# Performance work log

Measured on AMD Instinct MI355X. Metric: run time of the kernel, lower is better.

## Reference

```python
import jax, jax.numpy as jnp
import numpy as np

B, N, M, DK, DV, H = 4, 2048, 2048, 1024, 1024, 16
DKP = ((DK + H - 1) // H) * H  # 1024
DVP = ((DV + H - 1) // H) * H  # 1024


def setup_inputs() -> dict:
    key = jax.random.key(0)
    ks = jax.random.split(key, 12)
    s = 0.02
    return {
        "queries": jax.random.normal(ks[0], (B, N, DK), jnp.float32),
        "keys": jax.random.normal(ks[1], (B, M, DK), jnp.float32),
        "values": jax.random.normal(ks[2], (B, M, DV), jnp.float32),
        "presence": jnp.ones((B, M), jnp.float32),
        "n_heads": H,
        "wq": jax.random.normal(ks[3], (DK, DKP), jnp.float32) * s,
        "bq": jnp.zeros((DKP,), jnp.float32),
        "wk": jax.random.normal(ks[4], (DK, DKP), jnp.float32) * s,
        "bk": jnp.zeros((DKP,), jnp.float32),
        "wv": jax.random.normal(ks[5], (DV, DVP), jnp.float32) * s,
        "bv": jnp.zeros((DVP,), jnp.float32),
        "wo": jax.random.normal(ks[6], (DVP, DV), jnp.float32) * s,
        "bo": jnp.zeros((DV,), jnp.float32),
    }


def reference(queries, keys, values, presence, n_heads, wq, bq, wk, bk, wv, bv, wo, bo):
    b, n, _ = queries.shape
    m = keys.shape[1]
    h = n_heads
    # projections
    q = (queries @ wq + bq).reshape(b, n, h, -1)  # [B,N,H,dh]
    k = (keys @ wk + bk).reshape(b, m, h, -1)     # [B,M,H,dh]
    v = (values @ wv + bv).reshape(b, m, h, -1)   # [B,M,H,dv]
    dh = q.shape[-1]
    # scores: per-head scale is sqrt(per-head key dim), as in qkv_attention
    logits = jnp.einsum("bnhd,bmhd->bhnm", q, k)
    logits = logits - (1.0 - presence)[:, None, None, :] * 1e32
    attn = jax.nn.softmax(logits / jnp.sqrt(jnp.asarray(dh, logits.dtype)), axis=-1)
    o = jnp.einsum("bhnm,bmhd->bnhd", attn, v).reshape(b, n, -1)  # [B,N,DVP]
    return o @ wo + bo
```

## Files before the change

### kernel.cpp

```cpp
#include <hip/hip_runtime.h>


#define DI __device__ __forceinline__

typedef float f32x4 __attribute__((ext_vector_type(4)));
typedef __bf16 bf16x8 __attribute__((ext_vector_type(8)));
typedef __bf16 bf16x2 __attribute__((ext_vector_type(2)));
typedef unsigned short ushort8v __attribute__((ext_vector_type(8)));
typedef unsigned int uint4v __attribute__((ext_vector_type(4)));

typedef const __attribute__((address_space(1))) void gvoid_t;
typedef __attribute__((address_space(3))) void lvoid_t;

DI unsigned short f2b(float f) { return __builtin_bit_cast(unsigned short, (__bf16)f); }

DI unsigned pack2(float a, float b) {
  bf16x2 v;
  v[0] = (__bf16)a;
  v[1] = (__bf16)b;
  return __builtin_bit_cast(unsigned, v);
}

DI void swap32(unsigned& x, unsigned& y) {
  asm volatile("v_permlane32_swap_b32 %0, %1" : "+v"(x), "+v"(y));
}
DI void swap16(unsigned& x, unsigned& y) {
  asm volatile("v_permlane16_swap_b32 %0, %1" : "+v"(x), "+v"(y));
}

DI void gload16(const void* g, void* l) {
  __builtin_amdgcn_global_load_lds((gvoid_t*)g, (lvoid_t*)l, 16, 0, 0);
}

__global__ __launch_bounds__(256) void cvt3_kernel(const float* __restrict__ q,
                                                   const float* __restrict__ k,
                                                   const float* __restrict__ v,
                                                   unsigned short* __restrict__ qo,
                                                   unsigned short* __restrict__ ko,
                                                   unsigned short* __restrict__ vo) {
  const int z = blockIdx.y;
  const float* in = z == 0 ? q : z == 1 ? k : v;
  unsigned short* out = z == 0 ? qo : z == 1 ? ko : vo;
  int i = blockIdx.x * 256 + threadIdx.x;
  float4 vv = ((const float4*)in)[i];
  ushort4 o;
  o.x = f2b(vv.x); o.y = f2b(vv.y); o.z = f2b(vv.z); o.w = f2b(vv.w);
  ((ushort4*)out)[i] = o;
}

__global__ __launch_bounds__(256) void mask_kernel(const float* __restrict__ pres,
                                                   float* __restrict__ pm, int n) {
  int i = blockIdx.x * 256 + threadIdx.x;
  if (i < n) pm[i] = (pres[i] - 1.0f) * 1.8033688011112042e31f;
}

__global__ __launch_bounds__(256) void wtrans4_kernel(const float* __restrict__ w0,
                                                      const float* __restrict__ w1,
                                                      const float* __restrict__ w2,
                                                      const float* __restrict__ w3,
                                                      unsigned short* __restrict__ o0,
                                                      unsigned short* __restrict__ o1,
                                                      unsigned short* __restrict__ o2,
                                                      unsigned short* __restrict__ o3) {
  __shared__ float t[32][33];
  const int z = blockIdx.z;
  const float* in = z == 0 ? w0 : z == 1 ? w1 : z == 2 ? w2 : w3;
  unsigned short* out = z == 0 ? o0 : z == 1 ? o1 : z == 2 ? o2 : o3;
  const int n0 = blockIdx.x * 32, k0 = blockIdx.y * 32;
  const int tx = threadIdx.x, ty = threadIdx.y;
#pragma unroll
  for (int i = 0; i < 4; ++i)
    t[ty + i * 8][tx] = in[(size_t)(k0 + ty + i * 8) * 1024 + n0 + tx];
  __syncthreads();
#pragma unroll
  for (int i = 0; i < 4; ++i)
    out[(size_t)(n0 + ty + i * 8) * 1024 + k0 + tx] = f2b(t[tx][ty + i * 8]);
}


__global__ __launch_bounds__(256, 3) void gemm_qkv_kernel(
    const unsigned short* __restrict__ qin, const unsigned short* __restrict__ kin,
    const unsigned short* __restrict__ vin, const unsigned short* __restrict__ wqT,
    const unsigned short* __restrict__ wkT, const unsigned short* __restrict__ wvT,
    const float* __restrict__ bq, const float* __restrict__ bk,
    const float* __restrict__ bv, unsigned short* __restrict__ qb,
    unsigned short* __restrict__ kb, unsigned short* __restrict__ vTg) {
  __shared__ unsigned short ldsA[128 * 64];
  __shared__ unsigned short ldsB[128 * 64];

  const int z = blockIdx.z;
  const unsigned short* A = z == 0 ? qin : z == 1 ? kin : vin;
  const unsigned short* Bt = z == 0 ? wqT : z == 1 ? wkT : wvT;
  const float* bias = z == 0 ? bq : z == 1 ? bk : bv;

  const int nbx = 8;
  const int cpx = 64;
  const int wg0 = (int)blockIdx.x;
  const int wg = (wg0 & 7) * cpx + (wg0 >> 3);
  const int by = wg / nbx, bx = wg % nbx;

  const int tid = (int)threadIdx.x;
  const int w = tid >> 6, lane = tid & 63;
  const int lq = lane >> 4, lr = lane & 15;
  const int wr = w >> 1, wc = w & 1;

  const size_t rowA = (size_t)by * 128;
  const int colB = bx * 128;

  f32x4 acc[4][4];
#pragma unroll
  for (int m = 0; m < 4; ++m)
#pragma unroll
    for (int n = 0; n < 4; ++n) acc[m][n] = f32x4{0.f, 0.f, 0.f, 0.f};

  for (int k0 = 0; k0 < 1024; k0 += 64) {
#pragma unroll
    for (int i = 0; i < 4; ++i) {
      const int c = w * 4 + i;
      const int off = c * 1024 + lane * 16;
      const int row = off >> 7;
      const int kbs = (off & 127) ^ ((row & 7) << 4);
      gload16(A + ((rowA + row) * 1024 + k0 + (kbs >> 1)), &ldsA[c * 512]);
      gload16(Bt + ((size_t)(colB + row) * 1024 + k0 + (kbs >> 1)), &ldsB[c * 512]);
    }
    __syncthreads();
#pragma unroll
    for (int kk = 0; kk < 2; ++kk) {
      const int kbyte = kk * 64 + lq * 16;
      bf16x8 af[4], bfv[4];
#pragma unroll
      for (int m = 0; m < 4; ++m) {
        const int row = wr * 64 + m * 16 + lr;
        af[m] = *(const bf16x8*)((const char*)ldsA + row * 128 + (kbyte ^ ((row & 7) << 4)));
      }
#pragma unroll
      for (int n = 0; n < 4; ++n) {
        const int row = wc * 64 + n * 16 + lr;
        bfv[n] = *(const bf16x8*)((const char*)ldsB + row * 128 + (kbyte ^ ((row & 7) << 4)));
      }
#pragma unroll
      for (int m = 0; m < 4; ++m)
#pragma unroll
        for (int n = 0; n < 4; ++n)
          acc[m][n] = __builtin_amdgcn_mfma_f32_16x16x32_bf16(af[m], bfv[n], acc[m][n], 0, 0, 0);
    }
    __syncthreads();
  }

  if (z < 2) {
    unsigned short* C = z == 0 ? qb : kb;
#pragma unroll
    for (int n = 0; n < 4; ++n) {
      const int col = colB + wc * 64 + n * 16 + lr;
      const float bvl = bias[col];
#pragma unroll
      for (int m = 0; m < 4; ++m) {
        const size_t r0 = rowA + wr * 64 + m * 16 + lq * 4;
#pragma unroll
        for (int r = 0; r < 4; ++r) C[(r0 + r) * 1024 + col] = f2b(acc[m][n][r] + bvl);
      }
    }
  } else {
#pragma unroll
    for (int n = 0; n < 4; ++n) {
      const int col = colB + wc * 64 + n * 16 + lr;
      const float bvl = bias[col];
#pragma unroll
      for (int m = 0; m < 4; ++m) {
        const size_t row0 = rowA + wr * 64 + m * 16 + lq * 4;
        const int bb = (int)(row0 >> 11);
        const int ml = (int)(row0 & 2047);
        ushort4 o;
        o.x = f2b(acc[m][n][0] + bvl);
        o.y = f2b(acc[m][n][1] + bvl);
        o.z = f2b(acc[m][n][2] + bvl);
        o.w = f2b(acc[m][n][3] + bvl);
        *(ushort4*)(vTg + (((size_t)(bb * 1024 + col)) << 11) + ml) = o;
      }
    }
  }
}

__global__ __launch_bounds__(256, 3) void gemm_bt_kernel(const unsigned short* __restrict__ A,
                                                         const unsigned short* __restrict__ Bt,
                                                         const float* __restrict__ bias,
                                                         float* __restrict__ C) {
  __shared__ unsigned short ldsA[128 * 64];
  __shared__ unsigned short ldsB[128 * 64];

  const int nbx = 8;
  const int cpx = 64;
  const int wg0 = (int)blockIdx.x;
  const int wg = (wg0 & 7) * cpx + (wg0 >> 3);
  const int by = wg / nbx, bx = wg % nbx;

  const int tid = (int)threadIdx.x;
  const int w = tid >> 6, lane = tid & 63;
  const int lq = lane >> 4, lr = lane & 15;
  const int wr = w >> 1, wc = w & 1;

  const size_t rowA = (size_t)by * 128;
  const int colB = bx * 128;

  f32x4 acc[4][4];
#pragma unroll
  for (int m = 0; m < 4; ++m)
#pragma unroll
    for (int n = 0; n < 4; ++n) acc[m][n] = f32x4{0.f, 0.f, 0.f, 0.f};

  for (int k0 = 0; k0 < 1024; k0 += 64) {
#pragma unroll
    for (int i = 0; i < 4; ++i) {
      const int c = w * 4 + i;
      const int off = c * 1024 + lane * 16;
      const int row = off >> 7;
      const int kbs = (off & 127) ^ ((row & 7) << 4);
      gload16(A + ((rowA + row) * 1024 + k0 + (kbs >> 1)), &ldsA[c * 512]);
      gload16(Bt + ((size_t)(colB + row) * 1024 + k0 + (kbs >> 1)), &ldsB[c * 512]);
    }
    __syncthreads();
#pragma unroll
    for (int kk = 0; kk < 2; ++kk) {
      const int kbyte = kk * 64 + lq * 16;
      bf16x8 af[4], bfv[4];
#pragma unroll
      for (int m = 0; m < 4; ++m) {
        const int row = wr * 64 + m * 16 + lr;
        af[m] = *(const bf16x8*)((const char*)ldsA + row * 128 + (kbyte ^ ((row & 7) << 4)));
      }
#pragma unroll
      for (int n = 0; n < 4; ++n) {
        const int row = wc * 64 + n * 16 + lr;
        bfv[n] = *(const bf16x8*)((const char*)ldsB + row * 128 + (kbyte ^ ((row & 7) << 4)));
      }
#pragma unroll
      for (int m = 0; m < 4; ++m)
#pragma unroll
        for (int n = 0; n < 4; ++n)
          acc[m][n] = __builtin_amdgcn_mfma_f32_16x16x32_bf16(af[m], bfv[n], acc[m][n], 0, 0, 0);
    }
    __syncthreads();
  }

#pragma unroll
  for (int n = 0; n < 4; ++n) {
    const int col = colB + wc * 64 + n * 16 + lr;
    const float bvl = bias[col];
#pragma unroll
    for (int m = 0; m < 4; ++m) {
      const size_t r0 = rowA + wr * 64 + m * 16 + lq * 4;
#pragma unroll
      for (int r = 0; r < 4; ++r) C[(r0 + r) * 1024 + col] = acc[m][n][r] + bvl;
    }
  }
}

DI void softmax_pk(f32x4 s[4], float& mrun, float& lrun, f32x4 acc[4], unsigned* pk) {
  float rm = fmaxf(fmaxf(s[0][0], s[0][1]), fmaxf(s[0][2], s[0][3]));
#pragma unroll
  for (int kf = 1; kf < 4; ++kf)
    rm = fmaxf(rm, fmaxf(fmaxf(s[kf][0], s[kf][1]), fmaxf(s[kf][2], s[kf][3])));
  rm = fmaxf(rm, __shfl_xor(rm, 16, 64));
  rm = fmaxf(rm, __shfl_xor(rm, 32, 64));
  if (__any(rm > mrun + 8.0f)) {
    const float mn = fmaxf(mrun, rm);
    const float al = __builtin_amdgcn_exp2f(mrun - mn);
    lrun *= al;
#pragma unroll
    for (int df = 0; df < 4; ++df) acc[df] *= al;
    mrun = mn;
  }
  float rs = 0.f;
#pragma unroll
  for (int kf = 0; kf < 4; ++kf) {
#pragma unroll
    for (int r = 0; r < 4; ++r) {
      const float p = __builtin_amdgcn_exp2f(s[kf][r] - mrun);
      s[kf][r] = p;
      rs += p;
    }
    pk[kf * 2] = pack2(s[kf][0], s[kf][1]);
    pk[kf * 2 + 1] = pack2(s[kf][2], s[kf][3]);
  }
  rs += __shfl_xor(rs, 16, 64);
  rs += __shfl_xor(rs, 32, 64);
  lrun += rs;
}

DI bf16x8 pv_frag(const unsigned* pk, int kc) {
  unsigned x0 = pk[4 * kc + 0], y0 = pk[4 * kc + 2];
  swap32(x0, y0);
  swap16(x0, y0);
  unsigned x1 = pk[4 * kc + 1], y1 = pk[4 * kc + 3];
  swap32(x1, y1);
  swap16(x1, y1);
  uint4v wds;
  wds[0] = x0; wds[1] = x1; wds[2] = y0; wds[3] = y1;
  return __builtin_bit_cast(bf16x8, wds);
}

__global__ __launch_bounds__(256, 4) void attn_kernel(const unsigned short* __restrict__ Q,
                                                      const unsigned short* __restrict__ K,
                                                      const unsigned short* __restrict__ Vt,
                                                      const float* __restrict__ pm,
                                                      unsigned short* __restrict__ O) {
  __shared__ unsigned short kT[64 * 64];
  __shared__ unsigned short vT[64 * 64];

  const int q0 = blockIdx.x * 128;
  const int h = blockIdx.y, b = blockIdx.z;
  const int tid = (int)threadIdx.x;
  const int w = tid >> 6, lane = tid & 63;
  const int lq = lane >> 4, lr = lane & 15;

  const unsigned short* qp = Q + ((size_t)(b * 2048 + q0 + w * 32 + lr) * 1024 + h * 64);
  const bf16x8 qfA0 = *(const bf16x8*)(qp + lq * 8);
  const bf16x8 qfA1 = *(const bf16x8*)(qp + 32 + lq * 8);
  const bf16x8 qfB0 = *(const bf16x8*)(qp + 16384 + lq * 8);
  const bf16x8 qfB1 = *(const bf16x8*)(qp + 16384 + 32 + lq * 8);

  const int s7 = (lr & 7) << 4;
  const int rd0 = lr * 128 + ((lq * 16) ^ s7);
  const int rd1 = lr * 128 + ((64 + lq * 16) ^ s7);

  const int rowS0 = w * 16 + (lane >> 3), rowS1 = rowS0 + 8;
  const int colS0 = ((lane & 7) * 16) ^ ((rowS0 & 7) << 4);
  const int colS1 = ((lane & 7) * 16) ^ ((rowS1 & 7) << 4);
  const unsigned short* Kb = K + (size_t)(b * 2048) * 1024 + h * 64;
  const unsigned short* Vb = Vt + (size_t)((b * 16 + h) * 64) * 2048;
  const float* pmB = pm + b * 2048;

  f32x4 accA[4], accB[4];
#pragma unroll
  for (int df = 0; df < 4; ++df) {
    accA[df] = f32x4{0.f, 0.f, 0.f, 0.f};
    accB[df] = f32x4{0.f, 0.f, 0.f, 0.f};
  }
  float mA = -3.0e38f, lA = 0.f, mB = -3.0e38f, lB = 0.f;

  for (int m0 = 0; m0 < 2048; m0 += 64) {
    gload16(Kb + (size_t)(m0 + rowS0) * 1024 + (colS0 >> 1), &kT[(w * 2) * 512]);
    gload16(Vb + (size_t)rowS0 * 2048 + m0 + (colS0 >> 1), &vT[(w * 2) * 512]);
    gload16(Kb + (size_t)(m0 + rowS1) * 1024 + (colS1 >> 1), &kT[(w * 2 + 1) * 512]);
    gload16(Vb + (size_t)rowS1 * 2048 + m0 + (colS1 >> 1), &vT[(w * 2 + 1) * 512]);
    __syncthreads();

    f32x4 sA[4], sB[4];
#pragma unroll
    for (int kf = 0; kf < 4; ++kf) {
      sA[kf] = f32x4{0.f, 0.f, 0.f, 0.f};
      sB[kf] = f32x4{0.f, 0.f, 0.f, 0.f};
    }
#pragma unroll
    for (int kk = 0; kk < 2; ++kk) {
      const int rdk = kk ? rd1 : rd0;
      const bf16x8 qa = kk ? qfA1 : qfA0;
      const bf16x8 qb_ = kk ? qfB1 : qfB0;
#pragma unroll
      for (int kf = 0; kf < 4; ++kf) {
        const bf16x8 kfr = *(const bf16x8*)((const char*)kT + rdk + kf * 2048);
        sA[kf] = __builtin_amdgcn_mfma_f32_16x16x32_bf16(kfr, qa, sA[kf], 0, 0, 0);
        sB[kf] = __builtin_amdgcn_mfma_f32_16x16x32_bf16(kfr, qb_, sB[kf], 0, 0, 0);
      }
    }

    const float SC = 0.18033688011112042f;
#pragma unroll
    for (int kf = 0; kf < 4; ++kf) {
      const f32x4 pv = *(const f32x4*)(pmB + m0 + kf * 16 + lq * 4);
#pragma unroll
      for (int r = 0; r < 4; ++r) {
        sA[kf][r] = sA[kf][r] * SC + pv[r];
        sB[kf][r] = sB[kf][r] * SC + pv[r];
      }
    }

    unsigned pkA[8], pkB[8];
    softmax_pk(sA, mA, lA, accA, pkA);
    softmax_pk(sB, mB, lB, accB, pkB);

#pragma unroll
    for (int kc = 0; kc < 2; ++kc) {
      const int rdk = kc ? rd1 : rd0;
      const bf16x8 pa = pv_frag(pkA, kc);
      const bf16x8 pb = pv_frag(pkB, kc);
#pragma unroll
      for (int df = 0; df < 4; ++df) {
        const bf16x8 vf = *(const bf16x8*)((const char*)vT + rdk + df * 2048);
        accA[df] = __builtin_amdgcn_mfma_f32_16x16x32_bf16(vf, pa, accA[df], 0, 0, 0);
        accB[df] = __builtin_amdgcn_mfma_f32_16x16x32_bf16(vf, pb, accB[df], 0, 0, 0);
      }
    }
    __syncthreads();
  }

  const float rlA = __builtin_amdgcn_rcpf(lA);
  const float rlB = __builtin_amdgcn_rcpf(lB);
  unsigned short* Op = O + ((size_t)(b * 2048 + q0 + w * 32 + lr) * 1024 + h * 64);
#pragma unroll
  for (int df = 0; df < 4; ++df) {
    ushort4 oa, ob;
    oa.x = f2b(accA[df][0] * rlA); oa.y = f2b(accA[df][1] * rlA);
    oa.z = f2b(accA[df][2] * rlA); oa.w = f2b(accA[df][3] * rlA);
    ob.x = f2b(accB[df][0] * rlB); ob.y = f2b(accB[df][1] * rlB);
    ob.z = f2b(accB[df][2] * rlB); ob.w = f2b(accB[df][3] * rlB);
    *(ushort4*)(Op + df * 16 + lq * 4) = oa;
    *(ushort4*)(Op + 16384 + df * 16 + lq * 4) = ob;
  }
}

extern "C" void kernel_launch(void* const* d_in, const int* in_sizes, int n_in,
                              void* d_out, int out_size, void* d_ws, size_t ws_size,
                              hipStream_t stream) {
  const float* queries = (const float*)d_in[0];
  const float* keys = (const float*)d_in[1];
  const float* values = (const float*)d_in[2];
  const float* presence = (const float*)d_in[3];
  const float* wq = (const float*)d_in[5];
  const float* bq = (const float*)d_in[6];
  const float* wk = (const float*)d_in[7];
  const float* bk = (const float*)d_in[8];
  const float* wv = (const float*)d_in[9];
  const float* bv = (const float*)d_in[10];
  const float* wo = (const float*)d_in[11];
  const float* bo = (const float*)d_in[12];
  float* out = (float*)d_out;

  char* ws = (char*)d_ws;
  const size_t MB = 1048576;
  unsigned short* qin = (unsigned short*)(ws + 0 * MB);
  unsigned short* kin = (unsigned short*)(ws + 16 * MB);
  unsigned short* vin = (unsigned short*)(ws + 32 * MB);
  unsigned short* qb = (unsigned short*)(ws + 48 * MB);
  unsigned short* kb = (unsigned short*)(ws + 64 * MB);
  unsigned short* vTg = (unsigned short*)(ws + 80 * MB);
  unsigned short* wqT = (unsigned short*)(ws + 96 * MB);
  unsigned short* wkT = (unsigned short*)(ws + 98 * MB);
  unsigned short* wvT = (unsigned short*)(ws + 100 * MB);
  unsigned short* woT = (unsigned short*)(ws + 102 * MB);
  float* pmb = (float*)(ws + 104 * MB);

  mask_kernel<<<32, 256, 0, stream>>>(presence, pmb, 8192);
  cvt3_kernel<<<dim3(8192, 3), 256, 0, stream>>>(queries, keys, values, qin, kin, vin);
  wtrans4_kernel<<<dim3(32, 32, 4), dim3(32, 8), 0, stream>>>(wq, wk, wv, wo, wqT, wkT, wvT,
                                                              woT);
  gemm_qkv_kernel<<<dim3(512, 1, 3), 256, 0, stream>>>(qin, kin, vin, wqT, wkT, wvT, bq, bk,
                                                       bv, qb, kb, vTg);
  attn_kernel<<<dim3(16, 16, 4), 256, 0, stream>>>(qb, kb, vTg, pmb, qin);
  gemm_bt_kernel<<<512, 256, 0, stream>>>(qin, woT, bo, out);
}
```

Before: 374.7 us.

## Triple-buffer GEMM LDS staging with 256x128 tiles and 8 waves

Rewrites both projection GEMMs around a shared core that keeps three LDS stages in flight, issues the next-next tile's global->LDS loads interleaved with MFMAs, and syncs with a single barrier per k-step using vmcnt waits. The tile grows to 256x128 per block, with 512 threads (8 waves) and 144KB of LDS, and MFMA sections get a raised issue priority. The aim is to hide global load latency and halve barrier overhead. In exchange, occupancy is limited by LDS to one block per CU, and the grid shrinks to 256 blocks per GEMM (768 blocks across the three QKV projections).

```diff
diff --git a/kernel.cpp b/kernel.cpp
--- a/kernel.cpp
+++ b/kernel.cpp
@@ -77,85 +77,135 @@
     out[(size_t)(n0 + ty + i * 8) * 1024 + k0 + tx] = f2b(t[tx][ty + i * 8]);
 }
 
-
-__global__ __launch_bounds__(256, 3) void gemm_qkv_kernel(
+DI void stage_a_chunk(const unsigned short* A, size_t rowA, int k0, char* dst, int w,
+                      int lane, int i) {
+  const int c = w * 4 + i;
+  const int off = c * 1024 + lane * 16;
+  const int row = off >> 7;
+  const int cb = (off & 127) ^ ((row & 7) << 4);
+  gload16(A + (rowA + row) * 1024 + k0 + (cb >> 1), dst + c * 1024);
+}
+DI void stage_b_chunk(const unsigned short* Bt, int colB, int k0, char* dst, int w,
+                      int lane, int i) {
+  const int c = w * 2 + i;
+  const int off = c * 1024 + lane * 16;
+  const int row = off >> 7;
+  const int cb = (off & 127) ^ ((row & 7) << 4);
+  gload16(Bt + (size_t)(colB + row) * 1024 + k0 + (cb >> 1), dst + c * 1024);
+}
+
+DI void gemm_core(const unsigned short* __restrict__ A, const unsigned short* __restrict__ Bt,
+                  size_t rowA, int colB, char* lds, f32x4 acc[4][4]) {
+  const int tid = (int)threadIdx.x;
+  const int w = tid >> 6, lane = tid & 63;
+  const int lq = lane >> 4, lr = lane & 15;
+  const int wm = w >> 1, wn = w & 1;
+
+  char* const buf0 = lds;
+  char* const buf1 = lds + 49152;
+  char* const buf2 = lds + 98304;
+
+#pragma unroll
+  for (int m = 0; m < 4; ++m)
+#pragma unroll
+    for (int n = 0; n < 4; ++n) acc[m][n] = f32x4{0.f, 0.f, 0.f, 0.f};
+
+#pragma unroll
+  for (int i = 0; i < 4; ++i) stage_a_chunk(A, rowA, 0, buf0, w, lane, i);
+#pragma unroll
+  for (int i = 0; i < 2; ++i) stage_b_chunk(Bt, colB, 0, buf0 + 32768, w, lane, i);
+#pragma unroll
+  for (int i = 0; i < 4; ++i) stage_a_chunk(A, rowA, 64, buf1, w, lane, i);
+#pragma unroll
+  for (int i = 0; i < 2; ++i) stage_b_chunk(Bt, colB, 64, buf1 + 32768, w, lane, i);
+
+  for (int t = 0; t < 16; ++t) {
+    if (t < 15)
+      asm volatile("s_waitcnt vmcnt(6)" ::: "memory");
+    else
+      asm volatile("s_waitcnt vmcnt(0)" ::: "memory");
+    __builtin_amdgcn_s_barrier();
+    __builtin_amdgcn_sched_barrier(0);
+
+    const int ti = t % 3;
+    char* cur = ti == 0 ? buf0 : ti == 1 ? buf1 : buf2;
+    const int ni = (t + 2) % 3;
+    char* nxt = ni == 0 ? buf0 : ni == 1 ? buf1 : buf2;
+    const bool st = (t + 2) < 16;
+    const int kn = (t + 2) * 64;
+
+    bf16x8 bfr[4][2];
+#pragma unroll
+    for (int n = 0; n < 4; ++n) {
+      const int row = wn * 64 + n * 16 + lr;
+      const char* base = cur + 32768 + row * 128;
+      const int sw = (row & 7) << 4;
+      bfr[n][0] = *(const bf16x8*)(base + ((lq * 16) ^ sw));
+      bfr[n][1] = *(const bf16x8*)(base + ((64 + lq * 16) ^ sw));
+    }
+#pragma unroll
+    for (int m = 0; m < 4; ++m) {
+      const int row = wm * 64 + m * 16 + lr;
+      const char* base = cur + row * 128;
+      const int sw = (row & 7) << 4;
+      const bf16x8 af0 = *(const bf16x8*)(base + ((lq * 16) ^ sw));
+      const bf16x8 af1 = *(const bf16x8*)(base + ((64 + lq * 16) ^ sw));
+      if (st) {
+        if (m < 2) {
+          stage_a_chunk(A, rowA, kn, nxt, w, lane, m * 2);
+          stage_a_chunk(A, rowA, kn, nxt, w, lane, m * 2 + 1);
+        } else {
+          stage_b_chunk(Bt, colB, kn, nxt + 32768, w, lane, m - 2);
+        }
+      }
+      __builtin_amdgcn_s_setprio(1);
+#pragma unroll
+      for (int n = 0; n < 4; ++n) {
+        acc[m][n] = __builtin_amdgcn_mfma_f32_16x16x32_bf16(af0, bfr[n][0], acc[m][n], 0, 0, 0);
+        acc[m][n] = __builtin_amdgcn_mfma_f32_16x16x32_bf16(af1, bfr[n][1], acc[m][n], 0, 0, 0);
+      }
+      __builtin_amdgcn_s_setprio(0);
+    }
+  }
+}
+
+__global__ __launch_bounds__(512, 2) void gemm_qkv_kernel(
     const unsigned short* __restrict__ qin, const unsigned short* __restrict__ kin,
     const unsigned short* __restrict__ vin, const unsigned short* __restrict__ wqT,
     const unsigned short* __restrict__ wkT, const unsigned short* __restrict__ wvT,
     const float* __restrict__ bq, const float* __restrict__ bk,
     const float* __restrict__ bv, unsigned short* __restrict__ qb,
     unsigned short* __restrict__ kb, unsigned short* __restrict__ vTg) {
-  __shared__ unsigned short ldsA[128 * 64];
-  __shared__ unsigned short ldsB[128 * 64];
+  __shared__ char lds[147456];
 
   const int z = blockIdx.z;
   const unsigned short* A = z == 0 ? qin : z == 1 ? kin : vin;
   const unsigned short* Bt = z == 0 ? wqT : z == 1 ? wkT : wvT;
   const float* bias = z == 0 ? bq : z == 1 ? bk : bv;
 
-  const int nbx = 8;
-  const int cpx = 64;
   const int wg0 = (int)blockIdx.x;
-  const int wg = (wg0 & 7) * cpx + (wg0 >> 3);
-  const int by = wg / nbx, bx = wg % nbx;
+  const int wg = (wg0 & 7) * 32 + (wg0 >> 3);
+  const int by = wg >> 3, bx = wg & 7;
+  const size_t rowA = (size_t)by * 256;
+  const int colB = bx * 128;
 
   const int tid = (int)threadIdx.x;
   const int w = tid >> 6, lane = tid & 63;
   const int lq = lane >> 4, lr = lane & 15;
-  const int wr = w >> 1, wc = w & 1;
-
-  const size_t rowA = (size_t)by * 128;
-  const int colB = bx * 128;
+  const int wm = w >> 1, wn = w & 1;
 
   f32x4 acc[4][4];
-#pragma unroll
-  for (int m = 0; m < 4; ++m)
-#pragma unroll
-    for (int n = 0; n < 4; ++n) acc[m][n] = f32x4{0.f, 0.f, 0.f, 0.f};
-
-  for (int k0 = 0; k0 < 1024; k0 += 64) {
-#pragma unroll
-    for (int i = 0; i < 4; ++i) {
-      const int c = w * 4 + i;
-      const int off = c * 1024 + lane * 16;
-      const int row = off >> 7;
-      const int kbs = (off & 127) ^ ((row & 7) << 4);
-      gload16(A + ((rowA + row) * 1024 + k0 + (kbs >> 1)), &ldsA[c * 512]);
-      gload16(Bt + ((size_t)(colB + row) * 1024 + k0 + (kbs >> 1)), &ldsB[c * 512]);
-    }
-    __syncthreads();
-#pragma unroll
-    for (int kk = 0; kk < 2; ++kk) {
-      const int kbyte = kk * 64 + lq * 16;
-      bf16x8 af[4], bfv[4];
-#pragma unroll
-      for (int m = 0; m < 4; ++m) {
-        const int row = wr * 64 + m * 16 + lr;
-        af[m] = *(const bf16x8*)((const char*)ldsA + row * 128 + (kbyte ^ ((row & 7) << 4)));
-      }
-#pragma unroll
-      for (int n = 0; n < 4; ++n) {
-        const int row = wc * 64 + n * 16 + lr;
-        bfv[n] = *(const bf16x8*)((const char*)ldsB + row * 128 + (kbyte ^ ((row & 7) << 4)));
-      }
-#pragma unroll
-      for (int m = 0; m < 4; ++m)
-#pragma unroll
-        for (int n = 0; n < 4; ++n)
-          acc[m][n] = __builtin_amdgcn_mfma_f32_16x16x32_bf16(af[m], bfv[n], acc[m][n], 0, 0, 0);
-    }
-    __syncthreads();
-  }
+  gemm_core(A, Bt, rowA, colB, lds, acc);
 
   if (z < 2) {
     unsigned short* C = z == 0 ? qb : kb;
 #pragma unroll
     for (int n = 0; n < 4; ++n) {
-      const int col = colB + wc * 64 + n * 16 + lr;
+      const int col = colB + wn * 64 + n * 16 + lr;
       const float bvl = bias[col];
 #pragma unroll
       for (int m = 0; m < 4; ++m) {
-        const size_t r0 = rowA + wr * 64 + m * 16 + lq * 4;
+        const size_t r0 = rowA + wm * 64 + m * 16 + lq * 4;
 #pragma unroll
         for (int r = 0; r < 4; ++r) C[(r0 + r) * 1024 + col] = f2b(acc[m][n][r] + bvl);
       }
@@ -163,11 +213,11 @@
   } else {
 #pragma unroll
     for (int n = 0; n < 4; ++n) {
-      const int col = colB + wc * 64 + n * 16 + lr;
+      const int col = colB + wn * 64 + n * 16 + lr;
       const float bvl = bias[col];
 #pragma unroll
       for (int m = 0; m < 4; ++m) {
-        const size_t row0 = rowA + wr * 64 + m * 16 + lq * 4;
+        const size_t row0 = rowA + wm * 64 + m * 16 + lq * 4;
         const int bb = (int)(row0 >> 11);
         const int ml = (int)(row0 & 2047);
         ushort4 o;
@@ -181,74 +231,33 @@
   }
 }
 
-__global__ __launch_bounds__(256, 3) void gemm_bt_kernel(const unsigned short* __restrict__ A,
+__global__ __launch_bounds__(512, 2) void gemm_bt_kernel(const unsigned short* __restrict__ A,
                                                          const unsigned short* __restrict__ Bt,
                                                          const float* __restrict__ bias,
                                                          float* __restrict__ C) {
-  __shared__ unsigned short ldsA[128 * 64];
-  __shared__ unsigned short ldsB[128 * 64];
-
-  const int nbx = 8;
-  const int cpx = 64;
+  __shared__ char lds[147456];
+
   const int wg0 = (int)blockIdx.x;
-  const int wg = (wg0 & 7) * cpx + (wg0 >> 3);
-  const int by = wg / nbx, bx = wg % nbx;
+  const int wg = (wg0 & 7) * 32 + (wg0 >> 3);
+  const int by = wg >> 3, bx = wg & 7;
+  const size_t rowA = (size_t)by * 256;
+  const int colB = bx * 128;
 
   const int tid = (int)threadIdx.x;
   const int w = tid >> 6, lane = tid & 63;
   const int lq = lane >> 4, lr = lane & 15;
-  const int wr = w >> 1, wc = w & 1;
-
-  const size_t rowA = (size_t)by * 128;
-  const int colB = bx * 128;
+  const int wm = w >> 1, wn = w & 1;
 
   f32x4 acc[4][4];
-#pragma unroll
-  for (int m = 0; m < 4; ++m)
-#pragma unroll
-    for (int n = 0; n < 4; ++n) acc[m][n] = f32x4{0.f, 0.f, 0.f, 0.f};
-
-  for (int k0 = 0; k0 < 1024; k0 += 64) {
-#pragma unroll
-    for (int i = 0; i < 4; ++i) {
-      const int c = w * 4 + i;
-      const int off = c * 1024 + lane * 16;
-      const int row = off >> 7;
-      const int kbs = (off & 127) ^ ((row & 7) << 4);
-      gload16(A + ((rowA + row) * 1024 + k0 + (kbs >> 1)), &ldsA[c * 512]);
-      gload16(Bt + ((size_t)(colB + row) * 1024 + k0 + (kbs >> 1)), &ldsB[c * 512]);
-    }
-    __syncthreads();
-#pragma unroll
-    for (int kk = 0; kk < 2; ++kk) {
-      const int kbyte = kk * 64 + lq * 16;
-      bf16x8 af[4], bfv[4];
-#pragma unroll
-      for (int m = 0; m < 4; ++m) {
-        const int row = wr * 64 + m * 16 + lr;
-        af[m] = *(const bf16x8*)((const char*)ldsA + row * 128 + (kbyte ^ ((row & 7) << 4)));
-      }
-#pragma unroll
-      for (int n = 0; n < 4; ++n) {
-        const int row = wc * 64 + n * 16 + lr;
-        bfv[n] = *(const bf16x8*)((const char*)ldsB + row * 128 + (kbyte ^ ((row & 7) << 4)));
-      }
-#pragma unroll
-      for (int m = 0; m < 4; ++m)
-#pragma unroll
-        for (int n = 0; n < 4; ++n)
-          acc[m][n] = __builtin_amdgcn_mfma_f32_16x16x32_bf16(af[m], bfv[n], acc[m][n], 0, 0, 0);
-    }
-    __syncthreads();
-  }
+  gemm_core(A, Bt, rowA, colB, lds, acc);
 
 #pragma unroll
   for (int n = 0; n < 4; ++n) {
-    const int col = colB + wc * 64 + n * 16 + lr;
+    const int col = colB + wn * 64 + n * 16 + lr;
     const float bvl = bias[col];
 #pragma unroll
     for (int m = 0; m < 4; ++m) {
-      const size_t r0 = rowA + wr * 64 + m * 16 + lq * 4;
+      const size_t r0 = rowA + wm * 64 + m * 16 + lq * 4;
 #pragma unroll
       for (int r = 0; r < 4; ++r) C[(r0 + r) * 1024 + col] = acc[m][n][r] + bvl;
     }
@@ -444,8 +453,8 @@
   cvt3_kernel<<<dim3(8192, 3), 256, 0, stream>>>(queries, keys, values, qin, kin, vin);
   wtrans4_kernel<<<dim3(32, 32, 4), dim3(32, 8), 0, stream>>>(wq, wk, wv, wo, wqT, wkT, wvT,
                                                               woT);
-  gemm_qkv_kernel<<<dim3(512, 1, 3), 256, 0, stream>>>(qin, kin, vin, wqT, wkT, wvT, bq, bk,
+  gemm_qkv_kernel<<<dim3(256, 1, 3), 512, 0, stream>>>(qin, kin, vin, wqT, wkT, wvT, bq, bk,
                                                        bv, qb, kb, vTg);
   attn_kernel<<<dim3(16, 16, 4), 256, 0, stream>>>(qb, kb, vTg, pmb, qin);
-  gemm_bt_kernel<<<512, 256, 0, stream>>>(qin, woT, bo, out);
-}
+  gemm_bt_kernel<<<256, 512, 0, stream>>>(qin, woT, bo, out);
+}
```

Result: no change. 369.0 us (-1.5%).
